# Performance work log

Measured on AMD Instinct MI355X. Metric: run time of the kernel, lower is better.

## Reference

```python
import jax, jax.numpy as jnp
import numpy as np

B, L, D_MODEL, N_HEAD, D_K, D_V, VOCAB = 2, 1024, 512, 8, 64, 64, 64
TEMP = float(np.sqrt(D_K))
LN_EPS = 1e-5


def setup_inputs() -> dict:
    key = jax.random.key(0)
    ks = jax.random.split(key, 24)
    inp = {}
    inp['q'] = jax.random.normal(ks[0], (B, L, D_MODEL), jnp.float32)
    inp['k'] = jax.random.normal(ks[1], (B, L, D_MODEL), jnp.float32)
    inp['v'] = jax.random.normal(ks[2], (B, L, D_MODEL), jnp.float32)
    inp['mask'] = jax.random.uniform(ks[3], (B, L, L)) < 0.1
    # tf_f1 carries -1 (padding) positions; its sign defines tf_mask for ALL five features
    inp['tf_f1'] = jax.random.randint(ks[4], (B, L, L), -1, VOCAB, jnp.int32)
    inp['tf_f2'] = jax.random.randint(ks[5], (B, L, L), 0, VOCAB, jnp.int32)
    inp['tf_f3'] = jax.random.randint(ks[6], (B, L, L), 0, VOCAB, jnp.int32)
    inp['tf_f4'] = jax.random.randint(ks[7], (B, L, L), 0, VOCAB, jnp.int32)
    inp['tf_f5'] = jax.random.randint(ks[8], (B, L, L), 0, VOCAB, jnp.int32)
    s_qk = np.sqrt(2.0 / (D_MODEL + D_K))
    s_v = np.sqrt(2.0 / (D_MODEL + D_V))
    inp['w_q'] = jax.random.normal(ks[9], (D_MODEL, N_HEAD * D_K), jnp.float32) * s_qk
    inp['b_q'] = jnp.zeros((N_HEAD * D_K,), jnp.float32)
    inp['w_k'] = jax.random.normal(ks[10], (D_MODEL, N_HEAD * D_K), jnp.float32) * s_qk
    inp['b_k'] = jnp.zeros((N_HEAD * D_K,), jnp.float32)
    inp['w_v'] = jax.random.normal(ks[11], (D_MODEL, N_HEAD * D_V), jnp.float32) * s_v
    inp['b_v'] = jnp.zeros((N_HEAD * D_V,), jnp.float32)
    for i in range(5):
        inp[f'emb{i+1}'] = jax.random.normal(ks[12 + i], (VOCAB, N_HEAD), jnp.float32)
    fc_std = np.sqrt(2.0 / (N_HEAD * D_V + D_MODEL))
    inp['fc_w'] = jax.random.normal(ks[17], (N_HEAD * D_V, D_MODEL), jnp.float32) * fc_std
    inp['fc_b'] = jnp.zeros((D_MODEL,), jnp.float32)
    inp['ln_g'] = jnp.ones((D_MODEL,), jnp.float32)
    inp['ln_b'] = jnp.zeros((D_MODEL,), jnp.float32)
    return inp


def _bias(emb, tf, tf_mask):
    # (tf * mask).long() embedding lookup, zeroed where mask==0 -> [H, B, L, L]
    idx = (tf.astype(jnp.float32) * tf_mask).astype(jnp.int32)
    feat = emb[idx] * tf_mask[..., None]          # [B, L, L, H]
    return jnp.transpose(feat, (3, 0, 1, 2))      # [H, B, L, L]


def reference(q, k, v, mask, tf_f1, tf_f2, tf_f3, tf_f4, tf_f5,
              w_q, b_q, w_k, b_k, w_v, b_v,
              emb1, emb2, emb3, emb4, emb5,
              fc_w, fc_b, ln_g, ln_b):
    residual = q
    qh = (q @ w_q + b_q).reshape(B, L, N_HEAD, D_K)
    kh = (k @ w_k + b_k).reshape(B, L, N_HEAD, D_K)
    vh = (v @ w_v + b_v).reshape(B, L, N_HEAD, D_V)

    scores = jnp.einsum('blhd,bmhd->hblm', qh, kh)  # [H, B, Lq, Lk]
    tf_mask = (tf_f1 >= 0).astype(jnp.float32)      # [B, L, L] (from tf_f1 only, as in torch)
    scores = (scores
              + _bias(emb1, tf_f1, tf_mask)
              + _bias(emb2, tf_f2, tf_mask)
              + _bias(emb3, tf_f3, tf_mask)
              + _bias(emb4, tf_f4, tf_mask)
              + _bias(emb5, tf_f5, tf_mask)) / TEMP
    scores = jnp.where(mask[None], -jnp.inf, scores)
    attn = jax.nn.softmax(scores, axis=-1)          # [H, B, L, L]; dropout = identity (eval)

    out = jnp.einsum('hblm,bmhd->blhd', attn, vh).reshape(B, L, N_HEAD * D_V)
    out = out @ fc_w + fc_b                          # dropout = identity (eval)
    out = out + residual
    mu = jnp.mean(out, axis=-1, keepdims=True)
    var = jnp.mean((out - mu) ** 2, axis=-1, keepdims=True)
    out = (out - mu) * jax.lax.rsqrt(var + LN_EPS) * ln_g + ln_b
    return out, attn.reshape(N_HEAD * B, L, L)
```

## Files before the change

kernel.cpp:

```cpp
#include <hip/hip_runtime.h>
#include <math.h>

#define L_SEQ 1024
#define DMODEL 512
#define NHEAD 8
#define NB 2

typedef __attribute__((ext_vector_type(8))) short bf8;
typedef __attribute__((ext_vector_type(4))) float f4;

__device__ __forceinline__ short f2bf(float f) {
    unsigned u = __float_as_uint(f);
    unsigned r = u + 0x7FFF + ((u >> 16) & 1);
    return (short)(r >> 16);
}

__global__ __launch_bounds__(256) void cast_bf16_kernel(
    const float* __restrict__ src, short* __restrict__ dst, int n4)
{
    int i = blockIdx.x * 256 + threadIdx.x;
    if (i < n4) {
        float4 f = ((const float4*)src)[i];
        short4 o;
        o.x = f2bf(f.x); o.y = f2bf(f.y); o.z = f2bf(f.z); o.w = f2bf(f.w);
        ((short4*)dst)[i] = o;
    }
}

__global__ __launch_bounds__(256) void transpose_cast_kernel(
    const float* __restrict__ s0, const float* __restrict__ s1,
    const float* __restrict__ s2, const float* __restrict__ s3,
    short* __restrict__ d0, short* __restrict__ d1,
    short* __restrict__ d2, short* __restrict__ d3)
{
    const float* src; short* dst;
    switch (blockIdx.z) {
        case 0: src = s0; dst = d0; break;
        case 1: src = s1; dst = d1; break;
        case 2: src = s2; dst = d2; break;
        default: src = s3; dst = d3; break;
    }
    __shared__ float tile[32][33];
    const int tx = threadIdx.x, ty = threadIdx.y;
    const int x0 = blockIdx.x * 32, y0 = blockIdx.y * 32;
#pragma unroll
    for (int j = 0; j < 32; j += 8)
        tile[ty + j][tx] = src[(size_t)(y0 + ty + j) * 512 + x0 + tx];
    __syncthreads();
#pragma unroll
    for (int j = 0; j < 32; j += 8)
        dst[(size_t)(x0 + ty + j) * 512 + y0 + tx] = f2bf(tile[tx][ty + j]);
}

template<int MODE>
__global__ __launch_bounds__(256) void gemm_mfma_kernel(
    const short* __restrict__ A, const short* __restrict__ Bt,
    const float* __restrict__ bias, void* __restrict__ Cout)
{
    const int w = threadIdx.x >> 6, lane = threadIdx.x & 63;
    const int lr = lane & 15, lq = lane >> 4;
    const int m_base = blockIdx.y * 64 + w * 16;
    const int n_base = blockIdx.x * 64;

    f4 acc[4];
    const f4 zero = {0.f, 0.f, 0.f, 0.f};
#pragma unroll
    for (int nf = 0; nf < 4; ++nf) acc[nf] = zero;

    for (int k0 = 0; k0 < 512; k0 += 32) {
        bf8 a = *(const bf8*)(A + (size_t)(m_base + lr) * 512 + k0 + lq * 8);
#pragma unroll
        for (int nf = 0; nf < 4; ++nf) {
            bf8 b = *(const bf8*)(Bt + (size_t)(n_base + nf * 16 + lr) * 512 + k0 + lq * 8);
            acc[nf] = __builtin_amdgcn_mfma_f32_16x16x32_bf16(a, b, acc[nf], 0, 0, 0);
        }
    }

#pragma unroll
    for (int nf = 0; nf < 4; ++nf) {
        const int n = n_base + nf * 16 + lr;
        const float bv = bias[n];
        const int mrow = m_base + lq * 4;
#pragma unroll
        for (int r = 0; r < 4; ++r) {
            const float val = acc[nf][r] + bv;
            const int m = mrow + r;
            if (MODE == 0) {
                ((short*)Cout)[(size_t)m * 512 + n] = f2bf(val);
            } else if (MODE == 1) {
                const int bb = m >> 10, l = m & 1023;
                ((short*)Cout)[((size_t)bb * 512 + n) * 1024 + l] = f2bf(val);
            } else {
                ((float*)Cout)[(size_t)m * 512 + n] = val;
            }
        }
    }
}

__global__ __launch_bounds__(256) void scores_mfma_kernel(
    const short* __restrict__ qh, const short* __restrict__ kh,
    float* __restrict__ sc)
{
    const int z = blockIdx.z, h = z >> 1, b = z & 1;
    const int w = threadIdx.x >> 6, lane = threadIdx.x & 63;
    const int wr = w >> 1, wc = w & 1;
    const int lr = lane & 15, lq = lane >> 4;
    const int l0 = blockIdx.y * 128 + wr * 64;
    const int m0 = blockIdx.x * 128 + wc * 64;
    const int colb = h * 64 + lq * 8;
    const size_t base = (size_t)b * L_SEQ * DMODEL;

    bf8 afr[4][2], bfr[4][2];
#pragma unroll
    for (int i = 0; i < 4; ++i)
#pragma unroll
        for (int kk = 0; kk < 2; ++kk) {
            afr[i][kk] = *(const bf8*)(qh + base + (size_t)(l0 + i * 16 + lr) * 512 + colb + kk * 32);
            bfr[i][kk] = *(const bf8*)(kh + base + (size_t)(m0 + i * 16 + lr) * 512 + colb + kk * 32);
        }

    f4 acc[4][4];
    const f4 zero = {0.f, 0.f, 0.f, 0.f};
#pragma unroll
    for (int mt = 0; mt < 4; ++mt)
#pragma unroll
        for (int nt = 0; nt < 4; ++nt) acc[mt][nt] = zero;

#pragma unroll
    for (int kk = 0; kk < 2; ++kk)
#pragma unroll
        for (int mt = 0; mt < 4; ++mt)
#pragma unroll
            for (int nt = 0; nt < 4; ++nt)
                acc[mt][nt] = __builtin_amdgcn_mfma_f32_16x16x32_bf16(
                    afr[mt][kk], bfr[nt][kk], acc[mt][nt], 0, 0, 0);

    float* out = sc + (size_t)z * L_SEQ * L_SEQ;
#pragma unroll
    for (int mt = 0; mt < 4; ++mt)
#pragma unroll
        for (int nt = 0; nt < 4; ++nt)
#pragma unroll
            for (int r = 0; r < 4; ++r)
                out[(size_t)(l0 + mt * 16 + lq * 4 + r) * 1024 + m0 + nt * 16 + lr] = acc[mt][nt][r];
}

__global__ __launch_bounds__(256) void bias_softmax_kernel(
    float* __restrict__ attn,
    const int* __restrict__ mask,
    const int* __restrict__ tf1, const int* __restrict__ tf2,
    const int* __restrict__ tf3, const int* __restrict__ tf4,
    const int* __restrict__ tf5,
    const float* __restrict__ emb1, const float* __restrict__ emb2,
    const float* __restrict__ emb3, const float* __restrict__ emb4,
    const float* __restrict__ emb5)
{
    const int l = blockIdx.x, b = blockIdx.y, t = threadIdx.x;
    __shared__ float embs[5][NHEAD][64];
    __shared__ float s[NHEAD][L_SEQ];
    __shared__ float rinv[NHEAD];

    {
        const float* es[5] = {emb1, emb2, emb3, emb4, emb5};
        for (int i = t; i < 5 * 512; i += 256) {
            int j = i >> 9, rem = i & 511;
            int h = rem >> 6, idx = rem & 63;
            embs[j][h][idx] = es[j][idx * NHEAD + h];
        }
    }
    __syncthreads();

    const size_t rowbase = ((size_t)(b * L_SEQ + l)) * L_SEQ;
#pragma unroll
    for (int c = 0; c < 4; ++c) {
        const int m = (c << 8) + t;
        const int am  = mask[rowbase + m];
        const int t1v = tf1[rowbase + m];
        float bias8[NHEAD];
        if (t1v >= 0) {
            const int i2 = tf2[rowbase + m];
            const int i3 = tf3[rowbase + m];
            const int i4 = tf4[rowbase + m];
            const int i5 = tf5[rowbase + m];
#pragma unroll
            for (int h = 0; h < NHEAD; ++h)
                bias8[h] = embs[0][h][t1v] + embs[1][h][i2] + embs[2][h][i3]
                         + embs[3][h][i4] + embs[4][h][i5];
        } else {
#pragma unroll
            for (int h = 0; h < NHEAD; ++h) bias8[h] = 0.f;
        }
#pragma unroll
        for (int h = 0; h < NHEAD; ++h) {
            const float raw = attn[(((size_t)(h * NB + b)) * L_SEQ + l) * L_SEQ + m];
            s[h][m] = am ? -INFINITY : (raw + bias8[h]) * 0.125f;
        }
    }
    __syncthreads();

    {
        const int h = t >> 5, i = t & 31;
        float mx = -INFINITY;
        for (int m = i; m < L_SEQ; m += 32) mx = fmaxf(mx, s[h][m]);
#pragma unroll
        for (int off = 16; off; off >>= 1) mx = fmaxf(mx, __shfl_down(mx, off, 32));
        mx = __shfl(mx, 0, 32);
        float sm = 0.f;
        for (int m = i; m < L_SEQ; m += 32) {
            float e = __expf(s[h][m] - mx);
            s[h][m] = e;
            sm += e;
        }
#pragma unroll
        for (int off = 16; off; off >>= 1) sm += __shfl_down(sm, off, 32);
        if (i == 0) rinv[h] = 1.0f / sm;
    }
    __syncthreads();

    float inv[NHEAD];
#pragma unroll
    for (int h = 0; h < NHEAD; ++h) inv[h] = rinv[h];
    for (int m = t; m < L_SEQ; m += 256) {
#pragma unroll
        for (int h = 0; h < NHEAD; ++h)
            attn[(((size_t)(h * NB + b)) * L_SEQ + l) * L_SEQ + m] = s[h][m] * inv[h];
    }
}

__global__ __launch_bounds__(256) void av_mfma_kernel(
    const float* __restrict__ attn, const short* __restrict__ vht,
    short* __restrict__ pv)
{
    const int z = blockIdx.y, h = z >> 1, b = z & 1;
    const int w = threadIdx.x >> 6, lane = threadIdx.x & 63;
    const int lr = lane & 15, lq = lane >> 4;
    const int l0 = blockIdx.x * 128 + w * 32;
    const float* Ab = attn + (size_t)z * L_SEQ * L_SEQ;
    const short* Bb = vht + ((size_t)b * 512 + h * 64) * 1024;

    f4 acc[2][4];
    const f4 zero = {0.f, 0.f, 0.f, 0.f};
#pragma unroll
    for (int mt = 0; mt < 2; ++mt)
#pragma unroll
        for (int nt = 0; nt < 4; ++nt) acc[mt][nt] = zero;

    for (int k0 = 0; k0 < L_SEQ; k0 += 32) {
        bf8 a[2];
#pragma unroll
        for (int mt = 0; mt < 2; ++mt) {
            const float* p = Ab + (size_t)(l0 + mt * 16 + lr) * 1024 + k0 + lq * 8;
            float4 f0 = *(const float4*)p;
            float4 f1 = *(const float4*)(p + 4);
            bf8 tv;
            tv[0] = f2bf(f0.x); tv[1] = f2bf(f0.y); tv[2] = f2bf(f0.z); tv[3] = f2bf(f0.w);
            tv[4] = f2bf(f1.x); tv[5] = f2bf(f1.y); tv[6] = f2bf(f1.z); tv[7] = f2bf(f1.w);
            a[mt] = tv;
        }
#pragma unroll
        for (int nt = 0; nt < 4; ++nt) {
            bf8 bv = *(const bf8*)(Bb + (size_t)(nt * 16 + lr) * 1024 + k0 + lq * 8);
            acc[0][nt] = __builtin_amdgcn_mfma_f32_16x16x32_bf16(a[0], bv, acc[0][nt], 0, 0, 0);
            acc[1][nt] = __builtin_amdgcn_mfma_f32_16x16x32_bf16(a[1], bv, acc[1][nt], 0, 0, 0);
        }
    }

#pragma unroll
    for (int nt = 0; nt < 4; ++nt) {
        const int n = nt * 16 + lr;
#pragma unroll
        for (int mt = 0; mt < 2; ++mt) {
            const int rowb = l0 + mt * 16 + lq * 4;
#pragma unroll
            for (int r = 0; r < 4; ++r)
                pv[(size_t)(b * L_SEQ + rowb + r) * 512 + h * 64 + n] = f2bf(acc[mt][nt][r]);
        }
    }
}

__global__ __launch_bounds__(256) void ln_kernel(
    const float* __restrict__ x, const float* __restrict__ res,
    const float* __restrict__ g, const float* __restrict__ bvec,
    float* __restrict__ out)
{
    const int row = blockIdx.x;
    const int t = threadIdx.x;
    float2 xv = ((const float2*)(x + (size_t)row * DMODEL))[t];
    float2 rv = ((const float2*)(res + (size_t)row * DMODEL))[t];
    const float a = xv.x + rv.x;
    const float c = xv.y + rv.y;
    float s = a + c, sq = a * a + c * c;
#pragma unroll
    for (int off = 32; off; off >>= 1) {
        s  += __shfl_down(s, off);
        sq += __shfl_down(sq, off);
    }
    __shared__ float ssum[4], ssq[4];
    __shared__ float smu, srs;
    const int wid = t >> 6, lane = t & 63;
    if (lane == 0) { ssum[wid] = s; ssq[wid] = sq; }
    __syncthreads();
    if (t == 0) {
        float ts = ssum[0] + ssum[1] + ssum[2] + ssum[3];
        float tq = ssq[0] + ssq[1] + ssq[2] + ssq[3];
        float mu = ts * (1.0f / DMODEL);
        float var = tq * (1.0f / DMODEL) - mu * mu;
        smu = mu;
        srs = rsqrtf(var + 1e-5f);
    }
    __syncthreads();
    const float mu = smu, rs = srs;
    float2 gv = ((const float2*)g)[t];
    float2 bv = ((const float2*)bvec)[t];
    float2 o;
    o.x = (a - mu) * rs * gv.x + bv.x;
    o.y = (c - mu) * rs * gv.y + bv.y;
    ((float2*)(out + (size_t)row * DMODEL))[t] = o;
}

extern "C" void kernel_launch(void* const* d_in, const int* in_sizes, int n_in,
                              void* d_out, int out_size, void* d_ws, size_t ws_size,
                              hipStream_t stream)
{
    const float* q    = (const float*)d_in[0];
    const float* k    = (const float*)d_in[1];
    const float* v    = (const float*)d_in[2];
    const int*   mask = (const int*)d_in[3];
    const int*   tf1  = (const int*)d_in[4];
    const int*   tf2  = (const int*)d_in[5];
    const int*   tf3  = (const int*)d_in[6];
    const int*   tf4  = (const int*)d_in[7];
    const int*   tf5  = (const int*)d_in[8];
    const float* w_q  = (const float*)d_in[9];
    const float* b_q  = (const float*)d_in[10];
    const float* w_k  = (const float*)d_in[11];
    const float* b_k  = (const float*)d_in[12];
    const float* w_v  = (const float*)d_in[13];
    const float* b_v  = (const float*)d_in[14];
    const float* emb1 = (const float*)d_in[15];
    const float* emb2 = (const float*)d_in[16];
    const float* emb3 = (const float*)d_in[17];
    const float* emb4 = (const float*)d_in[18];
    const float* emb5 = (const float*)d_in[19];
    const float* fc_w = (const float*)d_in[20];
    const float* fc_b = (const float*)d_in[21];
    const float* ln_g = (const float*)d_in[22];
    const float* ln_b = (const float*)d_in[23];

    float* out  = (float*)d_out;
    float* attn = out + (size_t)NB * L_SEQ * DMODEL;

    char* wsb = (char*)d_ws;
    short* qb   = (short*)(wsb + 0);
    short* kb   = (short*)(wsb + (2u << 20));
    short* vb   = (short*)(wsb + (4u << 20));
    short* Wtq  = (short*)(wsb + (6u << 20));
    short* Wtk  = (short*)(wsb + (6u << 20) + (512u << 10));
    short* Wtv  = (short*)(wsb + (7u << 20));
    short* Wtfc = (short*)(wsb + (7u << 20) + (512u << 10));
    short* qh   = (short*)(wsb + (8u << 20));
    short* kh   = (short*)(wsb + (10u << 20));
    short* vht  = (short*)(wsb + (12u << 20));
    short* pv   = (short*)(wsb + (14u << 20));
    float* fco  = (float*)(wsb + (16u << 20));

    const int n4 = NB * L_SEQ * DMODEL / 4;

    cast_bf16_kernel<<<n4 / 256, 256, 0, stream>>>(q, qb, n4);
    cast_bf16_kernel<<<n4 / 256, 256, 0, stream>>>(k, kb, n4);
    cast_bf16_kernel<<<n4 / 256, 256, 0, stream>>>(v, vb, n4);

    transpose_cast_kernel<<<dim3(16, 16, 4), dim3(32, 8), 0, stream>>>(
        w_q, w_k, w_v, fc_w, Wtq, Wtk, Wtv, Wtfc);

    dim3 gproj(DMODEL / 64, NB * L_SEQ / 64);
    gemm_mfma_kernel<0><<<gproj, 256, 0, stream>>>(qb, Wtq, b_q, qh);
    gemm_mfma_kernel<0><<<gproj, 256, 0, stream>>>(kb, Wtk, b_k, kh);
    gemm_mfma_kernel<1><<<gproj, 256, 0, stream>>>(vb, Wtv, b_v, vht);

    scores_mfma_kernel<<<dim3(8, 8, 16), 256, 0, stream>>>(qh, kh, attn);

    bias_softmax_kernel<<<dim3(L_SEQ, NB), 256, 0, stream>>>(
        attn, mask, tf1, tf2, tf3, tf4, tf5, emb1, emb2, emb3, emb4, emb5);

    av_mfma_kernel<<<dim3(8, 16), 256, 0, stream>>>(attn, vht, pv);

    gemm_mfma_kernel<2><<<gproj, 256, 0, stream>>>(pv, Wtfc, fc_b, fco);

    ln_kernel<<<NB * L_SEQ, 256, 0, stream>>>(fco, q, ln_g, ln_b, out);
}
```

Measured before the change: 335.9 us.

## Fuse scores, bias-softmax and AV into one attention kernel; batch projection launches

Replaces the separate scores, bias+softmax and attn@V kernels with a single kernel. Each block computes QK^T for 16 query rows and two heads, adds the packed embedding bias, runs softmax in shared memory, writes attn once, and does the AV MFMA straight from LDS. The tf/mask indices are loaded once per block into packed registers and reused across both heads, and the raw scores no longer round-trip through global memory. The cast and QKV projection launches are merged into single launches. In exchange the kernel uses a large LDS tile (about 66 KB), which limits occupancy, and the grid is only 512 blocks.

Result: slower. 344.7 us (+2.6%).

```diff
diff --git a/kernel.cpp b/kernel.cpp
--- a/kernel.cpp
+++ b/kernel.cpp
@@ -5,6 +5,7 @@
 #define DMODEL 512
 #define NHEAD 8
 #define NB 2
+#define LP 1028
 
 typedef __attribute__((ext_vector_type(8))) short bf8;
 typedef __attribute__((ext_vector_type(4))) float f4;
@@ -15,16 +16,18 @@
     return (short)(r >> 16);
 }
 
-__global__ __launch_bounds__(256) void cast_bf16_kernel(
-    const float* __restrict__ src, short* __restrict__ dst, int n4)
-{
+__global__ __launch_bounds__(256) void cast3_bf16_kernel(
+    const float* __restrict__ q, const float* __restrict__ k,
+    const float* __restrict__ v,
+    short* __restrict__ qb, short* __restrict__ kb, short* __restrict__ vb)
+{
+    const float* src = (blockIdx.y == 0) ? q : (blockIdx.y == 1) ? k : v;
+    short* dst = (blockIdx.y == 0) ? qb : (blockIdx.y == 1) ? kb : vb;
     int i = blockIdx.x * 256 + threadIdx.x;
-    if (i < n4) {
-        float4 f = ((const float4*)src)[i];
-        short4 o;
-        o.x = f2bf(f.x); o.y = f2bf(f.y); o.z = f2bf(f.z); o.w = f2bf(f.w);
-        ((short4*)dst)[i] = o;
-    }
+    float4 f = ((const float4*)src)[i];
+    short4 o;
+    o.x = f2bf(f.x); o.y = f2bf(f.y); o.z = f2bf(f.z); o.w = f2bf(f.w);
+    ((short4*)dst)[i] = o;
 }
 
 __global__ __launch_bounds__(256) void transpose_cast_kernel(
@@ -52,10 +55,9 @@
         dst[(size_t)(x0 + ty + j) * 512 + y0 + tx] = f2bf(tile[tx][ty + j]);
 }
 
-template<int MODE>
-__global__ __launch_bounds__(256) void gemm_mfma_kernel(
+__device__ __forceinline__ void gemm_mfma_body(
     const short* __restrict__ A, const short* __restrict__ Bt,
-    const float* __restrict__ bias, void* __restrict__ Cout)
+    const float* __restrict__ bias, void* __restrict__ Cout, int mode)
 {
     const int w = threadIdx.x >> 6, lane = threadIdx.x & 63;
     const int lr = lane & 15, lq = lane >> 4;
@@ -85,9 +87,9 @@
         for (int r = 0; r < 4; ++r) {
             const float val = acc[nf][r] + bv;
             const int m = mrow + r;
-            if (MODE == 0) {
+            if (mode == 0) {
                 ((short*)Cout)[(size_t)m * 512 + n] = f2bf(val);
-            } else if (MODE == 1) {
+            } else if (mode == 1) {
                 const int bb = m >> 10, l = m & 1023;
                 ((short*)Cout)[((size_t)bb * 512 + n) * 1024 + l] = f2bf(val);
             } else {
@@ -97,183 +99,172 @@
     }
 }
 
-__global__ __launch_bounds__(256) void scores_mfma_kernel(
+__global__ __launch_bounds__(256) void qkv_proj_kernel(
+    const short* __restrict__ qb, const short* __restrict__ kb,
+    const short* __restrict__ vb,
+    const short* __restrict__ Wtq, const short* __restrict__ Wtk,
+    const short* __restrict__ Wtv,
+    const float* __restrict__ b_q, const float* __restrict__ b_k,
+    const float* __restrict__ b_v,
+    short* __restrict__ qh, short* __restrict__ kh, short* __restrict__ vht)
+{
+    if (blockIdx.z == 0)       gemm_mfma_body(qb, Wtq, b_q, qh, 0);
+    else if (blockIdx.z == 1)  gemm_mfma_body(kb, Wtk, b_k, kh, 0);
+    else                       gemm_mfma_body(vb, Wtv, b_v, vht, 1);
+}
+
+__global__ __launch_bounds__(256) void fc_kernel(
+    const short* __restrict__ A, const short* __restrict__ Bt,
+    const float* __restrict__ bias, float* __restrict__ C)
+{
+    gemm_mfma_body(A, Bt, bias, C, 2);
+}
+
+__global__ __launch_bounds__(256) void attn_fused_kernel(
     const short* __restrict__ qh, const short* __restrict__ kh,
-    float* __restrict__ sc)
-{
-    const int z = blockIdx.z, h = z >> 1, b = z & 1;
-    const int w = threadIdx.x >> 6, lane = threadIdx.x & 63;
-    const int wr = w >> 1, wc = w & 1;
-    const int lr = lane & 15, lq = lane >> 4;
-    const int l0 = blockIdx.y * 128 + wr * 64;
-    const int m0 = blockIdx.x * 128 + wc * 64;
-    const int colb = h * 64 + lq * 8;
-    const size_t base = (size_t)b * L_SEQ * DMODEL;
-
-    bf8 afr[4][2], bfr[4][2];
-#pragma unroll
-    for (int i = 0; i < 4; ++i)
-#pragma unroll
-        for (int kk = 0; kk < 2; ++kk) {
-            afr[i][kk] = *(const bf8*)(qh + base + (size_t)(l0 + i * 16 + lr) * 512 + colb + kk * 32);
-            bfr[i][kk] = *(const bf8*)(kh + base + (size_t)(m0 + i * 16 + lr) * 512 + colb + kk * 32);
-        }
-
-    f4 acc[4][4];
-    const f4 zero = {0.f, 0.f, 0.f, 0.f};
-#pragma unroll
-    for (int mt = 0; mt < 4; ++mt)
-#pragma unroll
-        for (int nt = 0; nt < 4; ++nt) acc[mt][nt] = zero;
-
-#pragma unroll
-    for (int kk = 0; kk < 2; ++kk)
-#pragma unroll
-        for (int mt = 0; mt < 4; ++mt)
-#pragma unroll
-            for (int nt = 0; nt < 4; ++nt)
-                acc[mt][nt] = __builtin_amdgcn_mfma_f32_16x16x32_bf16(
-                    afr[mt][kk], bfr[nt][kk], acc[mt][nt], 0, 0, 0);
-
-    float* out = sc + (size_t)z * L_SEQ * L_SEQ;
-#pragma unroll
-    for (int mt = 0; mt < 4; ++mt)
-#pragma unroll
-        for (int nt = 0; nt < 4; ++nt)
-#pragma unroll
-            for (int r = 0; r < 4; ++r)
-                out[(size_t)(l0 + mt * 16 + lq * 4 + r) * 1024 + m0 + nt * 16 + lr] = acc[mt][nt][r];
-}
-
-__global__ __launch_bounds__(256) void bias_softmax_kernel(
-    float* __restrict__ attn,
+    const short* __restrict__ vht,
     const int* __restrict__ mask,
     const int* __restrict__ tf1, const int* __restrict__ tf2,
     const int* __restrict__ tf3, const int* __restrict__ tf4,
     const int* __restrict__ tf5,
     const float* __restrict__ emb1, const float* __restrict__ emb2,
     const float* __restrict__ emb3, const float* __restrict__ emb4,
-    const float* __restrict__ emb5)
-{
-    const int l = blockIdx.x, b = blockIdx.y, t = threadIdx.x;
-    __shared__ float embs[5][NHEAD][64];
-    __shared__ float s[NHEAD][L_SEQ];
-    __shared__ float rinv[NHEAD];
-
-    {
-        const float* es[5] = {emb1, emb2, emb3, emb4, emb5};
-        for (int i = t; i < 5 * 512; i += 256) {
-            int j = i >> 9, rem = i & 511;
-            int h = rem >> 6, idx = rem & 63;
-            embs[j][h][idx] = es[j][idx * NHEAD + h];
+    const float* __restrict__ emb5,
+    float* __restrict__ attn, short* __restrict__ pv)
+{
+    const int hg = blockIdx.x;
+    const int l0 = blockIdx.y * 16;
+    const int b  = blockIdx.z;
+    const int t = threadIdx.x, w = t >> 6, lane = t & 63;
+    const int lq = lane >> 4, lr = lane & 15;
+
+    __shared__ float s[16 * LP];
+    __shared__ float embA[2][5][64];
+    __shared__ float redbuf[2][16][17];
+    __shared__ float rinvs[16];
+
+    for (int i = t; i < 640; i += 256) {
+        int hh = i / 320, rem = i % 320, j = rem >> 6, idx = rem & 63;
+        const float* ep = (j == 0) ? emb1 : (j == 1) ? emb2 : (j == 2) ? emb3
+                        : (j == 3) ? emb4 : emb5;
+        embA[hh][j][idx] = ep[idx * NHEAD + hg * 2 + hh];
+    }
+
+    unsigned packed[16][4];
+#pragma unroll
+    for (int r = 0; r < 4; ++r) {
+        const size_t posb = ((size_t)(b * L_SEQ + l0 + lq * 4 + r)) * L_SEQ + w * 256 + lr;
+#pragma unroll
+        for (int mt = 0; mt < 16; ++mt) {
+            const size_t pos = posb + mt * 16;
+            const int t1 = tf1[pos];
+            unsigned pk = mask[pos] ? 0x80000000u : 0u;
+            if (t1 >= 0) pk |= 0x40000000u | (unsigned)t1;
+            pk |= ((unsigned)tf2[pos]) << 6;
+            pk |= ((unsigned)tf3[pos]) << 12;
+            pk |= ((unsigned)tf4[pos]) << 18;
+            pk |= ((unsigned)tf5[pos]) << 24;
+            packed[mt][r] = pk;
         }
     }
     __syncthreads();
 
-    const size_t rowbase = ((size_t)(b * L_SEQ + l)) * L_SEQ;
-#pragma unroll
-    for (int c = 0; c < 4; ++c) {
-        const int m = (c << 8) + t;
-        const int am  = mask[rowbase + m];
-        const int t1v = tf1[rowbase + m];
-        float bias8[NHEAD];
-        if (t1v >= 0) {
-            const int i2 = tf2[rowbase + m];
-            const int i3 = tf3[rowbase + m];
-            const int i4 = tf4[rowbase + m];
-            const int i5 = tf5[rowbase + m];
-#pragma unroll
-            for (int h = 0; h < NHEAD; ++h)
-                bias8[h] = embs[0][h][t1v] + embs[1][h][i2] + embs[2][h][i3]
-                         + embs[3][h][i4] + embs[4][h][i5];
-        } else {
-#pragma unroll
-            for (int h = 0; h < NHEAD; ++h) bias8[h] = 0.f;
-        }
-#pragma unroll
-        for (int h = 0; h < NHEAD; ++h) {
-            const float raw = attn[(((size_t)(h * NB + b)) * L_SEQ + l) * L_SEQ + m];
-            s[h][m] = am ? -INFINITY : (raw + bias8[h]) * 0.125f;
-        }
-    }
-    __syncthreads();
-
-    {
-        const int h = t >> 5, i = t & 31;
-        float mx = -INFINITY;
-        for (int m = i; m < L_SEQ; m += 32) mx = fmaxf(mx, s[h][m]);
-#pragma unroll
-        for (int off = 16; off; off >>= 1) mx = fmaxf(mx, __shfl_down(mx, off, 32));
-        mx = __shfl(mx, 0, 32);
-        float sm = 0.f;
-        for (int m = i; m < L_SEQ; m += 32) {
-            float e = __expf(s[h][m] - mx);
-            s[h][m] = e;
-            sm += e;
-        }
-#pragma unroll
-        for (int off = 16; off; off >>= 1) sm += __shfl_down(sm, off, 32);
-        if (i == 0) rinv[h] = 1.0f / sm;
-    }
-    __syncthreads();
-
-    float inv[NHEAD];
-#pragma unroll
-    for (int h = 0; h < NHEAD; ++h) inv[h] = rinv[h];
-    for (int m = t; m < L_SEQ; m += 256) {
-#pragma unroll
-        for (int h = 0; h < NHEAD; ++h)
-            attn[(((size_t)(h * NB + b)) * L_SEQ + l) * L_SEQ + m] = s[h][m] * inv[h];
-    }
-}
-
-__global__ __launch_bounds__(256) void av_mfma_kernel(
-    const float* __restrict__ attn, const short* __restrict__ vht,
-    short* __restrict__ pv)
-{
-    const int z = blockIdx.y, h = z >> 1, b = z & 1;
-    const int w = threadIdx.x >> 6, lane = threadIdx.x & 63;
-    const int lr = lane & 15, lq = lane >> 4;
-    const int l0 = blockIdx.x * 128 + w * 32;
-    const float* Ab = attn + (size_t)z * L_SEQ * L_SEQ;
-    const short* Bb = vht + ((size_t)b * 512 + h * 64) * 1024;
-
-    f4 acc[2][4];
     const f4 zero = {0.f, 0.f, 0.f, 0.f};
-#pragma unroll
-    for (int mt = 0; mt < 2; ++mt)
-#pragma unroll
-        for (int nt = 0; nt < 4; ++nt) acc[mt][nt] = zero;
-
-    for (int k0 = 0; k0 < L_SEQ; k0 += 32) {
-        bf8 a[2];
-#pragma unroll
-        for (int mt = 0; mt < 2; ++mt) {
-            const float* p = Ab + (size_t)(l0 + mt * 16 + lr) * 1024 + k0 + lq * 8;
-            float4 f0 = *(const float4*)p;
-            float4 f1 = *(const float4*)(p + 4);
-            bf8 tv;
-            tv[0] = f2bf(f0.x); tv[1] = f2bf(f0.y); tv[2] = f2bf(f0.z); tv[3] = f2bf(f0.w);
-            tv[4] = f2bf(f1.x); tv[5] = f2bf(f1.y); tv[6] = f2bf(f1.z); tv[7] = f2bf(f1.w);
-            a[mt] = tv;
-        }
-#pragma unroll
-        for (int nt = 0; nt < 4; ++nt) {
-            bf8 bv = *(const bf8*)(Bb + (size_t)(nt * 16 + lr) * 1024 + k0 + lq * 8);
-            acc[0][nt] = __builtin_amdgcn_mfma_f32_16x16x32_bf16(a[0], bv, acc[0][nt], 0, 0, 0);
-            acc[1][nt] = __builtin_amdgcn_mfma_f32_16x16x32_bf16(a[1], bv, acc[1][nt], 0, 0, 0);
-        }
-    }
-
-#pragma unroll
-    for (int nt = 0; nt < 4; ++nt) {
-        const int n = nt * 16 + lr;
-#pragma unroll
-        for (int mt = 0; mt < 2; ++mt) {
-            const int rowb = l0 + mt * 16 + lq * 4;
-#pragma unroll
-            for (int r = 0; r < 4; ++r)
-                pv[(size_t)(b * L_SEQ + rowb + r) * 512 + h * 64 + n] = f2bf(acc[mt][nt][r]);
+
+    for (int hh = 0; hh < 2; ++hh) {
+        const int h = hg * 2 + hh;
+        if (hh) __syncthreads();
+
+        const short* qbase = qh + ((size_t)(b * L_SEQ + l0 + lr)) * 512 + h * 64 + lq * 8;
+        bf8 a0 = *(const bf8*)(qbase);
+        bf8 a1 = *(const bf8*)(qbase + 32);
+        f4 acc[16];
+#pragma unroll
+        for (int mt = 0; mt < 16; ++mt) acc[mt] = zero;
+        const short* kbase = kh + ((size_t)(b * L_SEQ + w * 256 + lr)) * 512 + h * 64 + lq * 8;
+#pragma unroll
+        for (int mt = 0; mt < 16; ++mt) {
+            bf8 b0 = *(const bf8*)(kbase + (size_t)mt * 16 * 512);
+            bf8 b1 = *(const bf8*)(kbase + (size_t)mt * 16 * 512 + 32);
+            acc[mt] = __builtin_amdgcn_mfma_f32_16x16x32_bf16(a0, b0, acc[mt], 0, 0, 0);
+            acc[mt] = __builtin_amdgcn_mfma_f32_16x16x32_bf16(a1, b1, acc[mt], 0, 0, 0);
+        }
+
+#pragma unroll
+        for (int mt = 0; mt < 16; ++mt) {
+#pragma unroll
+            for (int r = 0; r < 4; ++r) {
+                const unsigned pk = packed[mt][r];
+                float bias = 0.f;
+                if (pk & 0x40000000u)
+                    bias = embA[hh][0][pk & 63] + embA[hh][1][(pk >> 6) & 63]
+                         + embA[hh][2][(pk >> 12) & 63] + embA[hh][3][(pk >> 18) & 63]
+                         + embA[hh][4][(pk >> 24) & 63];
+                float val = (acc[mt][r] + bias) * 0.125f;
+                if (pk & 0x80000000u) val = -INFINITY;
+                s[(lq * 4 + r) * LP + w * 256 + mt * 16 + lr] = val;
+            }
+        }
+        __syncthreads();
+
+        const int srow = t & 15, cg = t >> 4;
+        {
+            float mx = -INFINITY;
+#pragma unroll 8
+            for (int j = 0; j < 64; ++j)
+                mx = fmaxf(mx, s[srow * LP + cg + 16 * j]);
+            redbuf[0][cg][srow] = mx;
+        }
+        __syncthreads();
+        float M = -INFINITY;
+#pragma unroll
+        for (int i = 0; i < 16; ++i) M = fmaxf(M, redbuf[0][i][srow]);
+        {
+            float sm = 0.f;
+#pragma unroll 8
+            for (int j = 0; j < 64; ++j) {
+                const int idx = srow * LP + cg + 16 * j;
+                float e = __expf(s[idx] - M);
+                s[idx] = e;
+                sm += e;
+            }
+            redbuf[1][cg][srow] = sm;
+        }
+        __syncthreads();
+        {
+            float tot = 0.f;
+#pragma unroll
+            for (int i = 0; i < 16; ++i) tot += redbuf[1][i][srow];
+            if (cg == 0) rinvs[srow] = 1.0f / tot;
+        }
+        __syncthreads();
+
+        float* abase = attn + (((size_t)(h * NB + b)) * L_SEQ + l0) * L_SEQ;
+#pragma unroll
+        for (int j = 0; j < 16; ++j) {
+            const float ri = rinvs[j];
+            float4 vv = *(float4*)&s[j * LP + 4 * t];
+            vv.x *= ri; vv.y *= ri; vv.z *= ri; vv.w *= ri;
+            *(float4*)&abase[(size_t)j * L_SEQ + 4 * t] = vv;
+        }
+
+        f4 pacc = zero;
+        const short* vbase = vht + ((size_t)(b * 512 + h * 64 + w * 16 + lr)) * L_SEQ + lq * 8;
+        for (int k0 = 0; k0 < L_SEQ; k0 += 32) {
+            const float* ap = &s[lr * LP + k0 + lq * 8];
+            float4 f0 = *(const float4*)ap;
+            float4 f1 = *(const float4*)(ap + 4);
+            bf8 af;
+            af[0] = f2bf(f0.x); af[1] = f2bf(f0.y); af[2] = f2bf(f0.z); af[3] = f2bf(f0.w);
+            af[4] = f2bf(f1.x); af[5] = f2bf(f1.y); af[6] = f2bf(f1.z); af[7] = f2bf(f1.w);
+            bf8 bf = *(const bf8*)(vbase + k0);
+            pacc = __builtin_amdgcn_mfma_f32_16x16x32_bf16(af, bf, pacc, 0, 0, 0);
+        }
+#pragma unroll
+        for (int r = 0; r < 4; ++r) {
+            const int row = lq * 4 + r;
+            const float o = pacc[r] * rinvs[row];
+            pv[((size_t)(b * L_SEQ + l0 + row)) * 512 + h * 64 + w * 16 + lr] = f2bf(o);
         }
     }
 }
@@ -366,26 +357,20 @@
 
     const int n4 = NB * L_SEQ * DMODEL / 4;
 
-    cast_bf16_kernel<<<n4 / 256, 256, 0, stream>>>(q, qb, n4);
-    cast_bf16_kernel<<<n4 / 256, 256, 0, stream>>>(k, kb, n4);
-    cast_bf16_kernel<<<n4 / 256, 256, 0, stream>>>(v, vb, n4);
+    cast3_bf16_kernel<<<dim3(n4 / 256, 3), 256, 0, stream>>>(q, k, v, qb, kb, vb);
 
     transpose_cast_kernel<<<dim3(16, 16, 4), dim3(32, 8), 0, stream>>>(
         w_q, w_k, w_v, fc_w, Wtq, Wtk, Wtv, Wtfc);
 
-    dim3 gproj(DMODEL / 64, NB * L_SEQ / 64);
-    gemm_mfma_kernel<0><<<gproj, 256, 0, stream>>>(qb, Wtq, b_q, qh);
-    gemm_mfma_kernel<0><<<gproj, 256, 0, stream>>>(kb, Wtk, b_k, kh);
-    gemm_mfma_kernel<1><<<gproj, 256, 0, stream>>>(vb, Wtv, b_v, vht);
-
-    scores_mfma_kernel<<<dim3(8, 8, 16), 256, 0, stream>>>(qh, kh, attn);
-
-    bias_softmax_kernel<<<dim3(L_SEQ, NB), 256, 0, stream>>>(
-        attn, mask, tf1, tf2, tf3, tf4, tf5, emb1, emb2, emb3, emb4, emb5);
-
-    av_mfma_kernel<<<dim3(8, 16), 256, 0, stream>>>(attn, vht, pv);
-
-    gemm_mfma_kernel<2><<<gproj, 256, 0, stream>>>(pv, Wtfc, fc_b, fco);
+    qkv_proj_kernel<<<dim3(DMODEL / 64, NB * L_SEQ / 64, 3), 256, 0, stream>>>(
+        qb, kb, vb, Wtq, Wtk, Wtv, b_q, b_k, b_v, qh, kh, vht);
+
+    attn_fused_kernel<<<dim3(4, 64, 2), 256, 0, stream>>>(
+        qh, kh, vht, mask, tf1, tf2, tf3, tf4, tf5,
+        emb1, emb2, emb3, emb4, emb5, attn, pv);
+
+    fc_kernel<<<dim3(DMODEL / 64, NB * L_SEQ / 64), 256, 0, stream>>>(
+        pv, Wtfc, fc_b, fco);
 
     ln_kernel<<<NB * L_SEQ, 256, 0, stream>>>(fco, q, ln_g, ln_b, out);
 }
```
